# Performance work log

Measured on AMD Instinct MI355X. Metric: run time of the kernel, lower is better.

Reference implementation:

```python
import jax, jax.numpy as jnp
import numpy as np

B, T, D, H, O = 32, 2048, 256, 512, 256


def setup_inputs() -> dict:
    key = jax.random.key(0)
    ks = jax.random.split(key, 8)
    s = lambda k, shp, fan: jax.random.normal(k, shp, dtype=jnp.float32) / np.sqrt(fan)
    return {
        "x": jax.random.normal(ks[0], (B, T, D), dtype=jnp.float32),
        "h0": jax.random.normal(ks[1], (1, B, H), dtype=jnp.float32),
        "W_ih": s(ks[2], (H, D), D),
        "W_hh": s(ks[3], (H, H), H),
        "b_ih": jnp.zeros((H,), jnp.float32),
        "b_hh": jnp.zeros((H,), jnp.float32),
        "W_lin": s(ks[4], (O, H), H),
        "b_lin": jnp.zeros((O,), jnp.float32),
    }


def reference(x, h0, W_ih, W_hh, b_ih, b_hh, W_lin, b_lin):
    # rnn_act == 'linear' branch: h_t = x_t @ W_ih^T + h_{t-1} @ W_hh^T + b_ih + b_hh
    h_init = h0[0]  # [B, H]
    # Precompute the input contribution for all timesteps at once: [B, T, H]
    xw = jnp.einsum("btd,hd->bth", x, W_ih) + (b_ih + b_hh)

    def step(h, xw_t):  # xw_t: [B, H]
        h_new = xw_t + h @ W_hh.T
        return h_new, h_new

    # scan over time axis
    _, z_t = jax.lax.scan(step, h_init, jnp.swapaxes(xw, 0, 1))  # [T, B, H]
    z = jnp.swapaxes(z_t, 0, 1)  # [B, T, H]

    logits = jnp.einsum("bth,oh->bto", z, W_lin) + b_lin
    out = jax.nn.softmax(logits, axis=2)
    return out, z
```

## Files before the change

kernel.cpp:

```cpp
#include <hip/hip_runtime.h>
#include <math.h>

#define B_ 32
#define T_ 2048
#define D_ 256
#define H_ 512
#define O_ 256
#define S_CH 8
#define C_CH 256

typedef short bf16x8 __attribute__((ext_vector_type(8)));
typedef float f32x4  __attribute__((ext_vector_type(4)));

#define NTL(p)     __builtin_nontemporal_load(p)

__device__ __forceinline__ unsigned short f2bf_rne(float x) {
    unsigned int u = __builtin_bit_cast(unsigned int, x);
    unsigned int r = (u + 0x7fffu + ((u >> 16) & 1u)) >> 16;
    return (unsigned short)r;
}
__device__ __forceinline__ float bf2f(unsigned short h) {
    unsigned int u = ((unsigned int)h) << 16;
    return __builtin_bit_cast(float, u);
}

#define MFMA16(a, b, c) __builtin_amdgcn_mfma_f32_16x16x32_bf16((a), (b), (c), 0, 0, 0)

__device__ __forceinline__ void split_frag(const float* p, bf16x8& hi, bf16x8& lo) {
    f32x4 a = *(const f32x4*)p;
    f32x4 b = *(const f32x4*)(p + 4);
#pragma unroll
    for (int i = 0; i < 4; i++) {
        unsigned short h = f2bf_rne(a[i]);
        hi[i] = (short)h; lo[i] = (short)f2bf_rne(a[i] - bf2f(h));
        unsigned short h2 = f2bf_rne(b[i]);
        hi[4 + i] = (short)h2; lo[4 + i] = (short)f2bf_rne(b[i] - bf2f(h2));
    }
}
__device__ __forceinline__ void split_frag_nt(const float* p, bf16x8& hi, bf16x8& lo) {
    f32x4 a = NTL((const f32x4*)p);
    f32x4 b = NTL((const f32x4*)(p + 4));
#pragma unroll
    for (int i = 0; i < 4; i++) {
        unsigned short h = f2bf_rne(a[i]);
        hi[i] = (short)h; lo[i] = (short)f2bf_rne(a[i] - bf2f(h));
        unsigned short h2 = f2bf_rne(b[i]);
        hi[4 + i] = (short)h2; lo[4 + i] = (short)f2bf_rne(b[i] - bf2f(h2));
    }
}

__device__ __forceinline__ size_t wpack_off(int n, int k, int KB) {
    int n16 = n >> 4, l15 = n & 15;
    int kb = k >> 5, lhi = (k >> 3) & 3, j = k & 7;
    return (((size_t)(n16 * KB + kb) * 4 + lhi) * 16 + l15) * 8 + j;
}

__device__ __forceinline__ int hfrag_off(int m, int n) {
    int m16 = m >> 4, l15m = m & 15;
    int kb = n >> 5, lhi = (n >> 3) & 3, j = n & 7;
    return (((m16 * 16 + kb) * 4 + lhi) * 16 + l15m) * 8 + j;
}

__global__ void k_pack(const float* __restrict__ in, unsigned short* __restrict__ hi,
                       unsigned short* __restrict__ lo, int total, int kshift) {
    int i = blockIdx.x * 256 + threadIdx.x;
    if (i < total) {
        int n = i >> kshift;
        int k = i & ((1 << kshift) - 1);
        float v = in[i];
        unsigned short h = f2bf_rne(v);
        size_t o = wpack_off(n, k, 1 << (kshift - 5));
        hi[o] = h;
        lo[o] = f2bf_rne(v - bf2f(h));
    }
}

__global__ __launch_bounds__(256) void k_mul(const float* __restrict__ A,
                                             const float* __restrict__ Bm,
                                             float* __restrict__ Out,
                                             unsigned short* __restrict__ d1h,
                                             unsigned short* __restrict__ d1l,
                                             unsigned short* __restrict__ d2h,
                                             unsigned short* __restrict__ d2l) {
    __shared__ float As[32][33];
    __shared__ float Bs[32][33];
    int tx = threadIdx.x & 15, ty = threadIdx.x >> 4;
    int j0 = blockIdx.x * 32, i0 = blockIdx.y * 32;
    float a00 = 0.f, a01 = 0.f, a10 = 0.f, a11 = 0.f;
    int r  = threadIdx.x >> 3;
    int c4 = (threadIdx.x & 7) * 4;
    for (int kb = 0; kb < H_ / 32; kb++) {
        f32x4 va = *(const f32x4*)(A + (size_t)(i0 + r) * H_ + kb * 32 + c4);
        f32x4 vb = *(const f32x4*)(Bm + (size_t)(kb * 32 + r) * H_ + j0 + c4);
        __syncthreads();
        As[r][c4 + 0] = va[0]; As[r][c4 + 1] = va[1]; As[r][c4 + 2] = va[2]; As[r][c4 + 3] = va[3];
        Bs[r][c4 + 0] = vb[0]; Bs[r][c4 + 1] = vb[1]; Bs[r][c4 + 2] = vb[2]; Bs[r][c4 + 3] = vb[3];
        __syncthreads();
#pragma unroll
        for (int k = 0; k < 32; k++) {
            float b0 = Bs[k][tx * 2], b1 = Bs[k][tx * 2 + 1];
            float a0 = As[ty * 2][k], a1 = As[ty * 2 + 1][k];
            a00 += a0 * b0; a01 += a0 * b1; a10 += a1 * b0; a11 += a1 * b1;
        }
    }
    float vals[4] = {a00, a01, a10, a11};
#pragma unroll
    for (int q = 0; q < 4; q++) {
        int n = i0 + ty * 2 + (q >> 1);
        int k = j0 + tx * 2 + (q & 1);
        Out[(size_t)n * H_ + k] = vals[q];
        unsigned short h = f2bf_rne(vals[q]);
        unsigned short l = f2bf_rne(vals[q] - bf2f(h));
        size_t o = wpack_off(n, k, 16);
        if (d1h) { d1h[o] = h; d1l[o] = l; }
        if (d2h) { d2h[o] = h; d2l[o] = l; }
    }
}

__global__ void k_seed(const float* __restrict__ h0, const float* __restrict__ zb,
                       float* __restrict__ Va) {
    int i = blockIdx.x * 256 + threadIdx.x;
    int c = i >> 14;
    int bn = i & 16383;
    int b = bn >> 9, n = bn & 511;
    Va[i] = (c == 0) ? h0[bn] : zb[((size_t)b * T_ + (c * S_CH - 1)) * H_ + n];
}

__global__ __launch_bounds__(1024) void k_scan2(const float* __restrict__ Vin,
                                                const unsigned short* __restrict__ Qp_hi,
                                                const unsigned short* __restrict__ Qp_lo,
                                                float* __restrict__ Vout, int s) {
    __shared__ __attribute__((aligned(16))) unsigned short hA[16384];
    __shared__ __attribute__((aligned(16))) unsigned short lA[16384];
    int c = blockIdx.x;
    int w = threadIdx.x >> 6;
    int lane = threadIdx.x & 63;
    int l15 = lane & 15, lhi = lane >> 4;

    if (c < s) {
        size_t base = (size_t)c * B_ * H_;
        for (int i = threadIdx.x * 4; i < B_ * H_; i += 4096) {
            f32x4 v = *(const f32x4*)(Vin + base + i);
            *(f32x4*)(Vout + base + i) = v;
        }
        return;
    }

    size_t src = (size_t)(c - s) * B_ * H_;
    for (int i = threadIdx.x; i < 16384; i += 1024) {
        float v = Vin[src + i];
        int m = i >> 9, n = i & 511;
        unsigned short hi = f2bf_rne(v);
        int o = hfrag_off(m, n);
        hA[o] = hi;
        lA[o] = f2bf_rne(v - bf2f(hi));
    }
    __syncthreads();

    size_t dst = (size_t)c * B_ * H_;
    float ad[2][2][4];
#pragma unroll
    for (int mt = 0; mt < 2; mt++)
#pragma unroll
        for (int nt = 0; nt < 2; nt++) {
            int n = w * 32 + nt * 16 + l15;
#pragma unroll
            for (int r = 0; r < 4; r++) {
                int m = mt * 16 + lhi * 4 + r;
                ad[mt][nt][r] = Vin[dst + (size_t)m * H_ + n];
            }
        }

    f32x4 acc[2][2];
#pragma unroll
    for (int mt = 0; mt < 2; mt++)
#pragma unroll
        for (int nt = 0; nt < 2; nt++) acc[mt][nt] = (f32x4){0.f, 0.f, 0.f, 0.f};

    for (int kb = 0; kb < 16; kb++) {
        bf16x8 ah0 = *(const bf16x8*)&hA[(kb << 9) + lane * 8];
        bf16x8 ah1 = *(const bf16x8*)&hA[((16 + kb) << 9) + lane * 8];
        bf16x8 al0 = *(const bf16x8*)&lA[(kb << 9) + lane * 8];
        bf16x8 al1 = *(const bf16x8*)&lA[((16 + kb) << 9) + lane * 8];
#pragma unroll
        for (int nt = 0; nt < 2; nt++) {
            size_t wb = (((size_t)(w * 2 + nt) * 16 + kb) << 9) + lane * 8;
            bf16x8 bh = *(const bf16x8*)(Qp_hi + wb);
            bf16x8 bl = *(const bf16x8*)(Qp_lo + wb);
            acc[0][nt] = MFMA16(ah0, bh, acc[0][nt]);
            acc[0][nt] = MFMA16(al0, bh, acc[0][nt]);
            acc[0][nt] = MFMA16(ah0, bl, acc[0][nt]);
            acc[1][nt] = MFMA16(ah1, bh, acc[1][nt]);
            acc[1][nt] = MFMA16(al1, bh, acc[1][nt]);
            acc[1][nt] = MFMA16(ah1, bl, acc[1][nt]);
        }
    }
#pragma unroll
    for (int mt = 0; mt < 2; mt++)
#pragma unroll
        for (int nt = 0; nt < 2; nt++) {
            int n = w * 32 + nt * 16 + l15;
#pragma unroll
            for (int r = 0; r < 4; r++) {
                int m = mt * 16 + lhi * 4 + r;
                Vout[dst + (size_t)m * H_ + n] = acc[mt][nt][r] + ad[mt][nt][r];
            }
        }
}

__global__ __launch_bounds__(512) void k_xw(const float* __restrict__ x,
                                            const unsigned short* __restrict__ Wp_hi,
                                            const unsigned short* __restrict__ Wp_lo,
                                            const float* __restrict__ bih,
                                            const float* __restrict__ bhh,
                                            float* __restrict__ zb) {
    int b  = blockIdx.y;
    int t0 = blockIdx.x * 64;
    int w    = threadIdx.x >> 6;
    int lane = threadIdx.x & 63;
    int l15 = lane & 15, lhi = lane >> 4;
    int nb = w * 64;

    f32x4 acc[4][4];
    for (int mt = 0; mt < 4; mt++)
        for (int nt = 0; nt < 4; nt++)
            acc[mt][nt] = (f32x4){0.f, 0.f, 0.f, 0.f};

    const float* xb = x + (size_t)b * T_ * D_;
    for (int kb = 0; kb < D_ / 32; kb++) {
        int kofs = kb * 32 + lhi * 8;
        bf16x8 ah[4], al[4];
#pragma unroll
        for (int mt = 0; mt < 4; mt++) {
            int t = t0 + mt * 16 + l15;
            split_frag_nt(xb + (size_t)t * D_ + kofs, ah[mt], al[mt]);
        }
#pragma unroll
        for (int nt = 0; nt < 4; nt++) {
            size_t wb = (((size_t)(w * 4 + nt) * 8 + kb) << 9) + lane * 8;
            bf16x8 bh = *(const bf16x8*)(Wp_hi + wb);
            bf16x8 bl = *(const bf16x8*)(Wp_lo + wb);
#pragma unroll
            for (int mt = 0; mt < 4; mt++) {
                acc[mt][nt] = MFMA16(ah[mt], bh, acc[mt][nt]);
                acc[mt][nt] = MFMA16(al[mt], bh, acc[mt][nt]);
                acc[mt][nt] = MFMA16(ah[mt], bl, acc[mt][nt]);
            }
        }
    }
#pragma unroll
    for (int nt = 0; nt < 4; nt++) {
        int n = nb + nt * 16 + l15;
        float bias = bih[n] + bhh[n];
#pragma unroll
        for (int mt = 0; mt < 4; mt++) {
#pragma unroll
            for (int r = 0; r < 4; r++) {
                int t = t0 + mt * 16 + lhi * 4 + r;
                zb[((size_t)b * T_ + t) * H_ + n] = acc[mt][nt][r] + bias;
            }
        }
    }
}

__global__ __launch_bounds__(1024) void k_phase1(const unsigned short* __restrict__ Wp_hi,
                                                 const unsigned short* __restrict__ Wp_lo,
                                                 float* __restrict__ zb) {
    __shared__ __attribute__((aligned(16))) unsigned short hA[16384];
    __shared__ __attribute__((aligned(16))) unsigned short lA[16384];
    int c = blockIdx.x;
    int w = threadIdx.x >> 6;
    int lane = threadIdx.x & 63;
    int l15 = lane & 15, lhi = lane >> 4;

    for (int j = 0; j < S_CH; j++) {
        int t = c * S_CH + j;
        float xw[2][2][4];
#pragma unroll
        for (int mt = 0; mt < 2; mt++)
#pragma unroll
            for (int nt = 0; nt < 2; nt++) {
                int n = w * 32 + nt * 16 + l15;
#pragma unroll
                for (int r = 0; r < 4; r++) {
                    int b = mt * 16 + lhi * 4 + r;
                    xw[mt][nt][r] = zb[((size_t)b * T_ + t) * H_ + n];
                }
            }
        f32x4 acc[2][2];
#pragma unroll
        for (int mt = 0; mt < 2; mt++)
#pragma unroll
            for (int nt = 0; nt < 2; nt++) acc[mt][nt] = (f32x4){0.f, 0.f, 0.f, 0.f};
        if (j > 0) {
            for (int kb = 0; kb < 16; kb++) {
                bf16x8 ah0 = *(const bf16x8*)&hA[(kb << 9) + lane * 8];
                bf16x8 ah1 = *(const bf16x8*)&hA[((16 + kb) << 9) + lane * 8];
                bf16x8 al0 = *(const bf16x8*)&lA[(kb << 9) + lane * 8];
                bf16x8 al1 = *(const bf16x8*)&lA[((16 + kb) << 9) + lane * 8];
#pragma unroll
                for (int nt = 0; nt < 2; nt++) {
                    size_t wb = (((size_t)(w * 2 + nt) * 16 + kb) << 9) + lane * 8;
                    bf16x8 bh = *(const bf16x8*)(Wp_hi + wb);
                    bf16x8 bl = *(const bf16x8*)(Wp_lo + wb);
                    acc[0][nt] = MFMA16(ah0, bh, acc[0][nt]);
                    acc[0][nt] = MFMA16(al0, bh, acc[0][nt]);
                    acc[0][nt] = MFMA16(ah0, bl, acc[0][nt]);
                    acc[1][nt] = MFMA16(ah1, bh, acc[1][nt]);
                    acc[1][nt] = MFMA16(al1, bh, acc[1][nt]);
                    acc[1][nt] = MFMA16(ah1, bl, acc[1][nt]);
                }
            }
        }
        __syncthreads();
#pragma unroll
        for (int mt = 0; mt < 2; mt++) {
#pragma unroll
            for (int nt = 0; nt < 2; nt++) {
                int n = w * 32 + nt * 16 + l15;
#pragma unroll
                for (int r = 0; r < 4; r++) {
                    int b = mt * 16 + lhi * 4 + r;
                    float v = acc[mt][nt][r] + xw[mt][nt][r];
                    zb[((size_t)b * T_ + t) * H_ + n] = v;
                    unsigned short hi = f2bf_rne(v);
                    int o = hfrag_off(b, n);
                    hA[o] = hi;
                    lA[o] = f2bf_rne(v - bf2f(hi));
                }
            }
        }
        __syncthreads();
    }
}

__global__ __launch_bounds__(512) void k_carry(const float* __restrict__ Hin,
                                               const unsigned short* __restrict__ Pp_hi,
                                               const unsigned short* __restrict__ Pp_lo,
                                               float* __restrict__ zb) {
    int bid = blockIdx.x;
    int swz = (bid & 7) * 128 + (bid >> 3);
    int npanel = swz >> 6;
    int mtile  = swz & 63;
    int w = threadIdx.x >> 6, lane = threadIdx.x & 63;
    int l15 = lane & 15, lhi = lane >> 4;
    int wm = w >> 2, wn = w & 3;
    int m0 = mtile * 128 + wm * 64;
    int n16base = npanel * 16 + wn * 4;

    f32x4 acc[4][4];
#pragma unroll
    for (int mt = 0; mt < 4; mt++)
#pragma unroll
        for (int nt = 0; nt < 4; nt++) acc[mt][nt] = (f32x4){0.f, 0.f, 0.f, 0.f};

    for (int kb = 0; kb < 16; kb++) {
        int kofs = kb * 32 + lhi * 8;
        bf16x8 ah[4], al[4];
#pragma unroll
        for (int mt = 0; mt < 4; mt++)
            split_frag(Hin + (size_t)(m0 + mt * 16 + l15) * H_ + kofs, ah[mt], al[mt]);
#pragma unroll
        for (int nt = 0; nt < 4; nt++) {
            size_t wb = (((size_t)(n16base + nt) * 16 + kb) << 9) + lane * 8;
            bf16x8 bh = *(const bf16x8*)(Pp_hi + wb);
            bf16x8 bl = *(const bf16x8*)(Pp_lo + wb);
#pragma unroll
            for (int mt = 0; mt < 4; mt++) {
                acc[mt][nt] = MFMA16(ah[mt], bh, acc[mt][nt]);
                acc[mt][nt] = MFMA16(al[mt], bh, acc[mt][nt]);
                acc[mt][nt] = MFMA16(ah[mt], bl, acc[mt][nt]);
            }
        }
    }
#pragma unroll
    for (int nt = 0; nt < 4; nt++) {
        int col = (n16base + nt) * 16 + l15;
        int j = col >> 9, n = col & 511;
#pragma unroll
        for (int mt = 0; mt < 4; mt++) {
#pragma unroll
            for (int r = 0; r < 4; r++) {
                int m = m0 + mt * 16 + lhi * 4 + r;
                int c = m >> 5, b = m & 31;
                size_t zi = ((size_t)b * T_ + (c * S_CH + j)) * H_ + n;
                zb[zi] += acc[mt][nt][r];
            }
        }
    }
}

__global__ __launch_bounds__(256) void k_logits(const float* __restrict__ zq,
                                                const unsigned short* __restrict__ Wp_hi,
                                                const float* __restrict__ blin,
                                                float* __restrict__ out) {
    size_t row0 = (size_t)blockIdx.x * 64;
    int w = threadIdx.x >> 6, lane = threadIdx.x & 63;
    int l15 = lane & 15, lhi = lane >> 4;

    f32x4 acc[16];
#pragma unroll
    for (int nt = 0; nt < 16; nt++) acc[nt] = (f32x4){0.f, 0.f, 0.f, 0.f};

    const float* arow = zq + (row0 + (size_t)w * 16 + l15) * H_;
    for (int kb = 0; kb < 16; kb++) {
        int kofs = kb * 32 + lhi * 8;
        bf16x8 ah, al;
        split_frag_nt(arow + kofs, ah, al);
#pragma unroll
        for (int nt = 0; nt < 16; nt++) {
            size_t wb = (((size_t)nt * 16 + kb) << 9) + lane * 8;
            bf16x8 bh = *(const bf16x8*)(Wp_hi + wb);
            acc[nt] = MFMA16(ah, bh, acc[nt]);
            acc[nt] = MFMA16(al, bh, acc[nt]);
        }
    }
#pragma unroll
    for (int nt = 0; nt < 16; nt++) {
        float bb = blin[nt * 16 + l15];
#pragma unroll
        for (int r = 0; r < 4; r++) acc[nt][r] += bb;
    }
    float rmax[4], rinv[4];
#pragma unroll
    for (int r = 0; r < 4; r++) {
        float mx = -INFINITY;
#pragma unroll
        for (int nt = 0; nt < 16; nt++) mx = fmaxf(mx, acc[nt][r]);
        for (int s = 1; s < 16; s <<= 1) mx = fmaxf(mx, __shfl_xor(mx, s));
        float sum = 0.f;
#pragma unroll
        for (int nt = 0; nt < 16; nt++) sum += __expf(acc[nt][r] - mx);
        for (int s = 1; s < 16; s <<= 1) sum += __shfl_xor(sum, s);
        rmax[r] = mx;
        rinv[r] = 1.f / sum;
    }
#pragma unroll
    for (int nt = 0; nt < 16; nt++) {
#pragma unroll
        for (int r = 0; r < 4; r++) {
            float e = __expf(acc[nt][r] - rmax[r]) * rinv[r];
            size_t row = row0 + (size_t)w * 16 + lhi * 4 + r;
            out[row * O_ + nt * 16 + l15] = e;
        }
    }
}

extern "C" void kernel_launch(void* const* d_in, const int* in_sizes, int n_in,
                              void* d_out, int out_size, void* d_ws, size_t ws_size,
                              hipStream_t stream) {
    const float* x    = (const float*)d_in[0];
    const float* h0   = (const float*)d_in[1];
    const float* Wih  = (const float*)d_in[2];
    const float* Whh  = (const float*)d_in[3];
    const float* bih  = (const float*)d_in[4];
    const float* bhh  = (const float*)d_in[5];
    const float* Wlin = (const float*)d_in[6];
    const float* blin = (const float*)d_in[7];

    float* out  = (float*)d_out;
    float* zout = out + (size_t)B_ * T_ * O_;

    float* ws = (float*)d_ws;
    float* M[14];
    for (int i = 0; i < 14; i++) M[i] = ws + (size_t)i * H_ * H_;
    unsigned short* Whh_hi = (unsigned short*)(ws + (size_t)14 * H_ * H_);
    unsigned short* Whh_lo = Whh_hi + (size_t)H_ * H_;
    unsigned short* Wih_hi = Whh_lo + (size_t)H_ * H_;
    unsigned short* Wih_lo = Wih_hi + (size_t)H_ * D_;
    unsigned short* Wlin_hi = Wih_lo + (size_t)H_ * D_;
    unsigned short* Wlin_lo = Wlin_hi + (size_t)O_ * H_;
    (void)Wlin_lo;

    float* Va = out;
    float* Vb = out + (size_t)C_CH * B_ * H_;
    unsigned short* Pp_hi = (unsigned short*)((char*)d_out + (size_t)32 * 1024 * 1024);
    unsigned short* Pp_lo = Pp_hi + (size_t)8 * H_ * H_;
    unsigned short* Qp_hi = Pp_lo + (size_t)8 * H_ * H_;
    unsigned short* Qp_lo = Qp_hi + (size_t)8 * H_ * H_;

    k_pack<<<dim3((H_ * H_) / 256), 256, 0, stream>>>(Whh, Whh_hi, Whh_lo, H_ * H_, 9);
    k_pack<<<dim3((H_ * H_) / 256), 256, 0, stream>>>(Whh, Pp_hi, Pp_lo, H_ * H_, 9);
    k_pack<<<dim3((H_ * D_) / 256), 256, 0, stream>>>(Wih, Wih_hi, Wih_lo, H_ * D_, 8);
    k_pack<<<dim3((O_ * H_) / 256), 256, 0, stream>>>(Wlin, Wlin_hi, Wlin_lo, O_ * H_, 9);

    dim3 g16(16, 16);
    size_t HH = (size_t)H_ * H_;
    unsigned short* nul = nullptr;
#define PPH(s) (Pp_hi + (size_t)(s) * HH)
#define PPL(s) (Pp_lo + (size_t)(s) * HH)
#define QPH(s) (Qp_hi + (size_t)(s) * HH)
#define QPL(s) (Qp_lo + (size_t)(s) * HH)
    k_mul<<<g16, 256, 0, stream>>>(Whh, Whh, M[0], PPH(1), PPL(1), nul, nul);
    k_mul<<<g16, 256, 0, stream>>>(Whh, M[0], M[1], PPH(2), PPL(2), nul, nul);
    k_mul<<<g16, 256, 0, stream>>>(M[0], M[0], M[2], PPH(3), PPL(3), nul, nul);
    k_mul<<<g16, 256, 0, stream>>>(Whh, M[2], M[3], PPH(4), PPL(4), nul, nul);
    k_mul<<<g16, 256, 0, stream>>>(M[0], M[2], M[4], PPH(5), PPL(5), nul, nul);
    k_mul<<<g16, 256, 0, stream>>>(M[1], M[2], M[5], PPH(6), PPL(6), nul, nul);
    k_mul<<<g16, 256, 0, stream>>>(M[2], M[2], M[6], PPH(7), PPL(7), QPH(0), QPL(0));
    for (int i = 7; i < 14; i++)
        k_mul<<<g16, 256, 0, stream>>>(M[i - 1], M[i - 1], M[i],
                                       QPH(i - 6), QPL(i - 6), nul, nul);
#undef PPH
#undef PPL
#undef QPH
#undef QPL

    k_xw<<<dim3(T_ / 64, B_), 512, 0, stream>>>(x, Wih_hi, Wih_lo, bih, bhh, zout);

    k_phase1<<<dim3(C_CH), 1024, 0, stream>>>(Whh_hi, Whh_lo, zout);

    k_seed<<<dim3((C_CH * B_ * H_) / 256), 256, 0, stream>>>(h0, zout, Va);
    {
        float* vin = Va;
        float* vout = Vb;
        int s = 1;
        for (int l = 0; l < 8; l++) {
            k_scan2<<<dim3(C_CH), 1024, 0, stream>>>(
                vin, Qp_hi + (size_t)l * HH, Qp_lo + (size_t)l * HH, vout, s);
            float* tmp = vin; vin = vout; vout = tmp;
            s <<= 1;
        }
    }

    k_carry<<<dim3(1024), 512, 0, stream>>>(Va, Pp_hi, Pp_lo, zout);

    k_logits<<<dim3((B_ * T_) / 64), 256, 0, stream>>>(zout, Wlin_hi, blin, out);
}
```

Before: 1.353 ms.

## Batch power-matrix multiplies, keep W_hh fragments in registers, re-swizzle carry tiles

Independent matrix-power products are grouped into two multi-z launches, cutting the number of serial kernel launches in the precompute chain. A redundant W_hh pack is dropped, and phase1 reuses the Pp slot 0 copy. k_phase1 now loads its per-wave W_hh hi/lo fragments into registers once and fully unrolls the k loop, avoiding repeated global loads across the eight timesteps. The k_carry block-to-tile mapping is also changed to group mtiles per XCD. The register preload adds 64 bf16x8 values per thread, which risks spills at 1024-thread launch bounds.

```diff
diff --git a/kernel.cpp b/kernel.cpp
--- a/kernel.cpp
+++ b/kernel.cpp
@@ -62,28 +62,30 @@
 }
 
 __global__ void k_pack(const float* __restrict__ in, unsigned short* __restrict__ hi,
-                       unsigned short* __restrict__ lo, int total, int kshift) {
+                       unsigned short* __restrict__ lo, unsigned short* __restrict__ hi2,
+                       unsigned short* __restrict__ lo2, int total, int kshift) {
     int i = blockIdx.x * 256 + threadIdx.x;
     if (i < total) {
         int n = i >> kshift;
         int k = i & ((1 << kshift) - 1);
         float v = in[i];
         unsigned short h = f2bf_rne(v);
+        unsigned short l = f2bf_rne(v - bf2f(h));
         size_t o = wpack_off(n, k, 1 << (kshift - 5));
         hi[o] = h;
-        lo[o] = f2bf_rne(v - bf2f(h));
-    }
-}
-
-__global__ __launch_bounds__(256) void k_mul(const float* __restrict__ A,
-                                             const float* __restrict__ Bm,
-                                             float* __restrict__ Out,
-                                             unsigned short* __restrict__ d1h,
-                                             unsigned short* __restrict__ d1l,
-                                             unsigned short* __restrict__ d2h,
-                                             unsigned short* __restrict__ d2l) {
-    __shared__ float As[32][33];
-    __shared__ float Bs[32][33];
+        lo[o] = l;
+        if (hi2) { hi2[o] = h; lo2[o] = l; }
+    }
+}
+
+__device__ __forceinline__ void mul_body(const float* __restrict__ A,
+                                         const float* __restrict__ Bm,
+                                         float* __restrict__ Out,
+                                         unsigned short* __restrict__ d1h,
+                                         unsigned short* __restrict__ d1l,
+                                         unsigned short* __restrict__ d2h,
+                                         unsigned short* __restrict__ d2l,
+                                         float (*As)[33], float (*Bs)[33]) {
     int tx = threadIdx.x & 15, ty = threadIdx.x >> 4;
     int j0 = blockIdx.x * 32, i0 = blockIdx.y * 32;
     float a00 = 0.f, a01 = 0.f, a10 = 0.f, a11 = 0.f;
@@ -117,6 +119,54 @@
     }
 }
 
+__global__ __launch_bounds__(256) void k_mul(const float* __restrict__ A,
+                                             const float* __restrict__ Bm,
+                                             float* __restrict__ Out,
+                                             unsigned short* __restrict__ d1h,
+                                             unsigned short* __restrict__ d1l,
+                                             unsigned short* __restrict__ d2h,
+                                             unsigned short* __restrict__ d2l) {
+    __shared__ float As[32][33];
+    __shared__ float Bs[32][33];
+    mul_body(A, Bm, Out, d1h, d1l, d2h, d2l, As, Bs);
+}
+
+__global__ __launch_bounds__(256) void k_mul_l2(const float* __restrict__ Whh,
+                                                float* __restrict__ ws,
+                                                unsigned short* __restrict__ Pp_hi,
+                                                unsigned short* __restrict__ Pp_lo) {
+    __shared__ float As[32][33];
+    __shared__ float Bs[32][33];
+    size_t HH = (size_t)H_ * H_;
+    if (blockIdx.z == 0)
+        mul_body(Whh, ws, ws + HH, Pp_hi + 2 * HH, Pp_lo + 2 * HH, nullptr, nullptr, As, Bs);
+    else
+        mul_body(ws, ws, ws + 2 * HH, Pp_hi + 3 * HH, Pp_lo + 3 * HH, nullptr, nullptr, As, Bs);
+}
+
+__global__ __launch_bounds__(256) void k_mul_l3(const float* __restrict__ Whh,
+                                                float* __restrict__ ws,
+                                                unsigned short* __restrict__ Pp_hi,
+                                                unsigned short* __restrict__ Pp_lo,
+                                                unsigned short* __restrict__ Qp_hi,
+                                                unsigned short* __restrict__ Qp_lo) {
+    __shared__ float As[32][33];
+    __shared__ float Bs[32][33];
+    size_t HH = (size_t)H_ * H_;
+    float* M0 = ws;
+    float* M1 = ws + HH;
+    float* M2 = ws + 2 * HH;
+    int z = blockIdx.z;
+    if (z == 0)
+        mul_body(Whh, M2, ws + 3 * HH, Pp_hi + 4 * HH, Pp_lo + 4 * HH, nullptr, nullptr, As, Bs);
+    else if (z == 1)
+        mul_body(M0, M2, ws + 4 * HH, Pp_hi + 5 * HH, Pp_lo + 5 * HH, nullptr, nullptr, As, Bs);
+    else if (z == 2)
+        mul_body(M1, M2, ws + 5 * HH, Pp_hi + 6 * HH, Pp_lo + 6 * HH, nullptr, nullptr, As, Bs);
+    else
+        mul_body(M2, M2, ws + 6 * HH, Pp_hi + 7 * HH, Pp_lo + 7 * HH, Qp_hi, Qp_lo, As, Bs);
+}
+
 __global__ void k_seed(const float* __restrict__ h0, const float* __restrict__ zb,
                        float* __restrict__ Va) {
     int i = blockIdx.x * 256 + threadIdx.x;
@@ -273,6 +323,16 @@
     int lane = threadIdx.x & 63;
     int l15 = lane & 15, lhi = lane >> 4;
 
+    bf16x8 wh[2][16], wl[2][16];
+#pragma unroll
+    for (int nt = 0; nt < 2; nt++)
+#pragma unroll
+        for (int kb = 0; kb < 16; kb++) {
+            size_t wb = (((size_t)(w * 2 + nt) * 16 + kb) << 9) + lane * 8;
+            wh[nt][kb] = *(const bf16x8*)(Wp_hi + wb);
+            wl[nt][kb] = *(const bf16x8*)(Wp_lo + wb);
+        }
+
     for (int j = 0; j < S_CH; j++) {
         int t = c * S_CH + j;
         float xw[2][2][4];
@@ -293,6 +353,7 @@
 #pragma unroll
             for (int nt = 0; nt < 2; nt++) acc[mt][nt] = (f32x4){0.f, 0.f, 0.f, 0.f};
         if (j > 0) {
+#pragma unroll
             for (int kb = 0; kb < 16; kb++) {
                 bf16x8 ah0 = *(const bf16x8*)&hA[(kb << 9) + lane * 8];
                 bf16x8 ah1 = *(const bf16x8*)&hA[((16 + kb) << 9) + lane * 8];
@@ -300,15 +361,12 @@
                 bf16x8 al1 = *(const bf16x8*)&lA[((16 + kb) << 9) + lane * 8];
 #pragma unroll
                 for (int nt = 0; nt < 2; nt++) {
-                    size_t wb = (((size_t)(w * 2 + nt) * 16 + kb) << 9) + lane * 8;
-                    bf16x8 bh = *(const bf16x8*)(Wp_hi + wb);
-                    bf16x8 bl = *(const bf16x8*)(Wp_lo + wb);
-                    acc[0][nt] = MFMA16(ah0, bh, acc[0][nt]);
-                    acc[0][nt] = MFMA16(al0, bh, acc[0][nt]);
-                    acc[0][nt] = MFMA16(ah0, bl, acc[0][nt]);
-                    acc[1][nt] = MFMA16(ah1, bh, acc[1][nt]);
-                    acc[1][nt] = MFMA16(al1, bh, acc[1][nt]);
-                    acc[1][nt] = MFMA16(ah1, bl, acc[1][nt]);
+                    acc[0][nt] = MFMA16(ah0, wh[nt][kb], acc[0][nt]);
+                    acc[0][nt] = MFMA16(al0, wh[nt][kb], acc[0][nt]);
+                    acc[0][nt] = MFMA16(ah0, wl[nt][kb], acc[0][nt]);
+                    acc[1][nt] = MFMA16(ah1, wh[nt][kb], acc[1][nt]);
+                    acc[1][nt] = MFMA16(al1, wh[nt][kb], acc[1][nt]);
+                    acc[1][nt] = MFMA16(ah1, wl[nt][kb], acc[1][nt]);
                 }
             }
         }
@@ -339,9 +397,10 @@
                                                const unsigned short* __restrict__ Pp_lo,
                                                float* __restrict__ zb) {
     int bid = blockIdx.x;
-    int swz = (bid & 7) * 128 + (bid >> 3);
-    int npanel = swz >> 6;
-    int mtile  = swz & 63;
+    int xcd = bid & 7;
+    int idx = bid >> 3;
+    int mtile  = xcd * 8 + (idx & 7);
+    int npanel = idx >> 3;
     int w = threadIdx.x >> 6, lane = threadIdx.x & 63;
     int l15 = lane & 15, lhi = lane >> 4;
     int wm = w >> 2, wn = w & 3;
@@ -462,53 +521,42 @@
     float* zout = out + (size_t)B_ * T_ * O_;
 
     float* ws = (float*)d_ws;
-    float* M[14];
-    for (int i = 0; i < 14; i++) M[i] = ws + (size_t)i * H_ * H_;
-    unsigned short* Whh_hi = (unsigned short*)(ws + (size_t)14 * H_ * H_);
-    unsigned short* Whh_lo = Whh_hi + (size_t)H_ * H_;
-    unsigned short* Wih_hi = Whh_lo + (size_t)H_ * H_;
-    unsigned short* Wih_lo = Wih_hi + (size_t)H_ * D_;
+    size_t HH = (size_t)H_ * H_;
+    float* M13 = ws + (size_t)13 * HH;
+    unsigned short* Wih_hi  = (unsigned short*)(ws + (size_t)14 * HH);
+    unsigned short* Wih_lo  = Wih_hi + (size_t)H_ * D_;
     unsigned short* Wlin_hi = Wih_lo + (size_t)H_ * D_;
     unsigned short* Wlin_lo = Wlin_hi + (size_t)O_ * H_;
-    (void)Wlin_lo;
 
     float* Va = out;
     float* Vb = out + (size_t)C_CH * B_ * H_;
     unsigned short* Pp_hi = (unsigned short*)((char*)d_out + (size_t)32 * 1024 * 1024);
-    unsigned short* Pp_lo = Pp_hi + (size_t)8 * H_ * H_;
-    unsigned short* Qp_hi = Pp_lo + (size_t)8 * H_ * H_;
-    unsigned short* Qp_lo = Qp_hi + (size_t)8 * H_ * H_;
-
-    k_pack<<<dim3((H_ * H_) / 256), 256, 0, stream>>>(Whh, Whh_hi, Whh_lo, H_ * H_, 9);
-    k_pack<<<dim3((H_ * H_) / 256), 256, 0, stream>>>(Whh, Pp_hi, Pp_lo, H_ * H_, 9);
-    k_pack<<<dim3((H_ * D_) / 256), 256, 0, stream>>>(Wih, Wih_hi, Wih_lo, H_ * D_, 8);
-    k_pack<<<dim3((O_ * H_) / 256), 256, 0, stream>>>(Wlin, Wlin_hi, Wlin_lo, O_ * H_, 9);
+    unsigned short* Pp_lo = Pp_hi + (size_t)8 * HH;
+    unsigned short* Qp_hi = Pp_lo + (size_t)8 * HH;
+    unsigned short* Qp_lo = Qp_hi + (size_t)8 * HH;
+
+    unsigned short* nul = nullptr;
+
+    k_pack<<<dim3((H_ * H_) / 256), 256, 0, stream>>>(Whh, Pp_hi, Pp_lo, nul, nul, H_ * H_, 9);
+    k_pack<<<dim3((H_ * D_) / 256), 256, 0, stream>>>(Wih, Wih_hi, Wih_lo, nul, nul, H_ * D_, 8);
+    k_pack<<<dim3((O_ * H_) / 256), 256, 0, stream>>>(Wlin, Wlin_hi, Wlin_lo, nul, nul, O_ * H_, 9);
 
     dim3 g16(16, 16);
-    size_t HH = (size_t)H_ * H_;
-    unsigned short* nul = nullptr;
-#define PPH(s) (Pp_hi + (size_t)(s) * HH)
-#define PPL(s) (Pp_lo + (size_t)(s) * HH)
 #define QPH(s) (Qp_hi + (size_t)(s) * HH)
 #define QPL(s) (Qp_lo + (size_t)(s) * HH)
-    k_mul<<<g16, 256, 0, stream>>>(Whh, Whh, M[0], PPH(1), PPL(1), nul, nul);
-    k_mul<<<g16, 256, 0, stream>>>(Whh, M[0], M[1], PPH(2), PPL(2), nul, nul);
-    k_mul<<<g16, 256, 0, stream>>>(M[0], M[0], M[2], PPH(3), PPL(3), nul, nul);
-    k_mul<<<g16, 256, 0, stream>>>(Whh, M[2], M[3], PPH(4), PPL(4), nul, nul);
-    k_mul<<<g16, 256, 0, stream>>>(M[0], M[2], M[4], PPH(5), PPL(5), nul, nul);
-    k_mul<<<g16, 256, 0, stream>>>(M[1], M[2], M[5], PPH(6), PPL(6), nul, nul);
-    k_mul<<<g16, 256, 0, stream>>>(M[2], M[2], M[6], PPH(7), PPL(7), QPH(0), QPL(0));
+    k_mul<<<g16, 256, 0, stream>>>(Whh, Whh, ws, Pp_hi + HH, Pp_lo + HH, nul, nul);
+    k_mul_l2<<<dim3(16, 16, 2), 256, 0, stream>>>(Whh, ws, Pp_hi, Pp_lo);
+    k_mul_l3<<<dim3(16, 16, 4), 256, 0, stream>>>(Whh, ws, Pp_hi, Pp_lo, Qp_hi, Qp_lo);
     for (int i = 7; i < 14; i++)
-        k_mul<<<g16, 256, 0, stream>>>(M[i - 1], M[i - 1], M[i],
-                                       QPH(i - 6), QPL(i - 6), nul, nul);
-#undef PPH
-#undef PPL
+        k_mul<<<g16, 256, 0, stream>>>(ws + (size_t)(i - 1) * HH, ws + (size_t)(i - 1) * HH,
+                                       ws + (size_t)i * HH, QPH(i - 6), QPL(i - 6), nul, nul);
 #undef QPH
 #undef QPL
+    (void)M13;
 
     k_xw<<<dim3(T_ / 64, B_), 512, 0, stream>>>(x, Wih_hi, Wih_lo, bih, bhh, zout);
 
-    k_phase1<<<dim3(C_CH), 1024, 0, stream>>>(Whh_hi, Whh_lo, zout);
+    k_phase1<<<dim3(C_CH), 1024, 0, stream>>>(Pp_hi, Pp_lo, zout);
 
     k_seed<<<dim3((C_CH * B_ * H_) / 256), 256, 0, stream>>>(h0, zout, Va);
     {
```

After: 1.470 ms. 8.6% more time.
